# Kernel optimization log

Hardware: AMD Instinct MI355X
Metric: run time of the kernel (lower is better)

Reference implementation:

```python
import jax, jax.numpy as jnp
import numpy as np

B, N, D = 4, 2048, 1024
H, S, C, NSH, MV = 8, 3, 32, 3, 4


def _lin(key, fan_in, fan_out):
    k1, k2 = jax.random.split(key)
    lim = 1.0 / np.sqrt(fan_in)
    W = jax.random.uniform(k1, (fan_in, fan_out), minval=-lim, maxval=lim)
    b = jax.random.uniform(k2, (fan_out,), minval=-lim, maxval=lim)
    return W, b


def setup_inputs() -> dict:
    key = jax.random.key(0)
    ks = jax.random.split(key, 16)
    x = jax.random.normal(ks[0], (B, N, D), dtype=jnp.float32)
    W_sense, b_sense = _lin(ks[1], D, S * D)
    W_ctx, b_ctx = _lin(ks[2], D, D)
    W_sel, b_sel = _lin(ks[3], 2 * D, S)
    W_charge, b_charge = _lin(ks[4], D, 1)
    W_shell, b_shell = _lin(ks[5], D, NSH)
    W_class, b_class = _lin(ks[6], D, C)
    W_mass, b_mass = _lin(ks[7], D, 1)
    W_val, b_val = _lin(ks[8], D, MV)
    sparsity = 0.4
    init_val = -np.log(1.0 / sparsity - 1.0)
    compat_logits = jax.random.normal(ks[9], (C, C)) * 0.5 + init_val
    W_v, b_v = _lin(ks[10], D, D)
    W_out, b_out = _lin(ks[11], D, D)
    return {
        'x': x,
        'W_sense': W_sense, 'b_sense': b_sense,
        'W_ctx': W_ctx, 'b_ctx': b_ctx,
        'W_sel': W_sel, 'b_sel': b_sel,
        'W_charge': W_charge, 'b_charge': b_charge,
        'W_shell': W_shell, 'b_shell': b_shell,
        'W_class': W_class, 'b_class': b_class,
        'W_mass': W_mass, 'b_mass': b_mass,
        'W_val': W_val, 'b_val': b_val,
        'compat_logits': compat_logits.astype(jnp.float32),
        'w_charge': jnp.float32(1.0), 'w_shell': jnp.float32(0.5),
        'w_distance': jnp.float32(1.0), 'w_mass': jnp.float32(0.3),
        'w_valence': jnp.float32(0.3), 'temperature': jnp.float32(1.0),
        'W_v': W_v, 'b_v': b_v,
        'W_out': W_out, 'b_out': b_out,
    }


def reference(x, W_sense, b_sense, W_ctx, b_ctx, W_sel, b_sel,
              W_charge, b_charge, W_shell, b_shell, W_class, b_class,
              W_mass, b_mass, W_val, b_val, compat_logits,
              w_charge, w_shell, w_distance, w_mass, w_valence, temperature,
              W_v, b_v, W_out, b_out):
    b, n, d = x.shape
    sp = jax.nn.softplus

    # --- isotope selection (word-sense mixing) ---
    senses = (x @ W_sense + b_sense).reshape(b, n, S, d)          # (B,N,S,D)
    ctx_avg = (x @ W_ctx + b_ctx).mean(axis=1, keepdims=True)     # (B,1,D)
    sel_in = jnp.concatenate([x, jnp.broadcast_to(ctx_avg, (b, n, d))], axis=-1)
    sense_w = jax.nn.softmax(sel_in @ W_sel + b_sel, axis=-1)     # (B,N,S)
    x = jnp.einsum('bns,bnsd->bnd', sense_w, senses)

    # --- atomic properties ---
    charge = jnp.tanh(x @ W_charge + b_charge)[..., 0]            # (B,N)
    shell = jax.nn.softmax(x @ W_shell + b_shell, axis=-1)        # (B,N,NSH)
    cls = jnp.argmax(x @ W_class + b_class, axis=-1)              # (B,N) int
    mass = sp(x @ W_mass + b_mass)[..., 0] + 0.5                  # (B,N)
    val = jax.nn.softmax(x @ W_val + b_val, axis=-1)              # (B,N,MV)

    # --- class compatibility mask (B,N,N) ---
    compat = jax.nn.sigmoid((compat_logits + compat_logits.T) * 0.5)
    sparse_mask = compat[cls[:, :, None], cls[:, None, :]]

    # --- pairwise physics energy (B,N,N) ---
    pos = jnp.arange(n, dtype=x.dtype)
    dist = jnp.abs(pos[:, None] - pos[None, :])                   # (N,N)
    val_sum = val.sum(axis=-1)                                    # (B,N)
    E = (sp(w_charge) * charge[:, :, None] * charge[:, None, :]
         + sp(w_shell) * jnp.abs(shell[:, :, None, :] - shell[:, None, :, :]).sum(-1)
         - sp(w_distance) / (1.0 + 0.1 * dist)
         + sp(w_mass) * 0.1 * mass[:, :, None] * mass[:, None, :]
         - sp(w_valence) * (val_sum[:, :, None] + val_sum[:, None, :]) * 0.5)

    temp = sp(temperature)
    scores = (-E / temp) * sparse_mask
    causal = jnp.triu(jnp.ones((n, n), dtype=bool), k=1)
    scores = jnp.where(causal[None], -jnp.inf, scores)
    attn = jax.nn.softmax(scores, axis=-1)                        # (B,N,N)

    # --- weighted value aggregation (shared attn across heads) ---
    V = (x @ W_v + b_v).reshape(b, n, H, d // H)
    out = jnp.einsum('bij,bjhd->bihd', attn, V).reshape(b, n, d)
    return out @ W_out + b_out
```

## Files before the change

### kernel.cpp

```cpp
#include <hip/hip_runtime.h>
#include <hip/hip_bf16.h>
#include <cmath>

typedef __hip_bfloat16 bf16;
typedef __attribute__((ext_vector_type(4))) float floatx4;
typedef __attribute__((ext_vector_type(8))) short short8;
typedef __attribute__((ext_vector_type(8))) unsigned short ushort8;

__device__ __forceinline__ float bf2f(bf16 v) { return __bfloat162float(v); }
__device__ __forceinline__ bf16 f2bf(float v) { return __float2bfloat16(v); }
__device__ __forceinline__ float bfu2f(unsigned short u) { return __uint_as_float(((unsigned)u) << 16); }
__device__ __forceinline__ unsigned short f2bfu(float v) {
  bf16 h = __float2bfloat16(v);
  return __builtin_bit_cast(unsigned short, h);
}
__device__ __forceinline__ float softplusf(float x) {
  return x > 20.0f ? x : log1pf(expf(x));
}

__device__ __forceinline__ void async16(const void* g, void* l) {
  __builtin_amdgcn_global_load_lds(
      (const __attribute__((address_space(1))) unsigned int*)g,
      (__attribute__((address_space(3))) unsigned int*)l, 16, 0, 0);
}

template<int MODE, int CAUSAL, int ACCUM, int SWZ, int KSPLIT = 1>
__global__ __launch_bounds__(256) void gemm_bt(
    const bf16* __restrict__ A, const bf16* __restrict__ Bt,
    const float* __restrict__ bias, void* __restrict__ Cptr,
    int M, int N, int K, int lda, int ldb, int ldc,
    long aoffz, long boffz, long coffz)
{
  __shared__ __align__(16) bf16 As[2][128 * 64];
  __shared__ __align__(16) bf16 Bs[2][128 * 64];

  const int tid = threadIdx.x;
  const int lane = tid & 63;
  const int wave = tid >> 6;
  const int wr = wave >> 1, wc = wave & 1;
  const long z = blockIdx.z;
  int kstart = 0;
  long zz = z;
  if (KSPLIT > 1) {
    kstart = (int)(z % KSPLIT) * K;
    zz = z / KSPLIT;
  }
  A += zz * aoffz;
  Bt += zz * boffz;

  int bx, by;
  if (SWZ) {
    const int mtiles = M >> 7;
    const int per = mtiles >> 3;
    const int bid = (int)blockIdx.x;
    const int xcd = bid & 7;
    const int slot = bid >> 3;
    by = xcd * per + (slot % per);
    bx = slot / per;
  } else {
    bx = blockIdx.x;
    by = blockIdx.y;
  }
  const int m0 = by * 128, n0 = bx * 128;
  int kend = kstart + K;
  if (CAUSAL) {
    int klim = (by + 1) * 128;
    if (klim < kend) kend = klim;
  }

  int aoff[4], boff[4];
#pragma unroll
  for (int q = 0; q < 4; q++) {
    int ch = tid + 256 * q;
    int r = ch >> 3, c4 = ch & 7;
    int scol = (c4 ^ (r & 7)) * 8;
    aoff[q] = (m0 + r) * lda + scol;
    boff[q] = (n0 + r) * ldb + scol;
  }

  floatx4 acc[4][4] = {};
  const int fm = lane & 15, fq = lane >> 4;

  const int nt = (kend - kstart) >> 6;

#pragma unroll
  for (int q = 0; q < 4; q++) {
    int ch8 = (tid + 256 * q) * 8;
    async16(&A[(size_t)aoff[q] + kstart], &As[0][ch8]);
    async16(&Bt[(size_t)boff[q] + kstart], &Bs[0][ch8]);
  }
  __syncthreads();

  int cur = 0;
  for (int t = 0; t < nt; t++) {
    if (t + 1 < nt) {
      const int k0 = kstart + (t + 1) * 64;
#pragma unroll
      for (int q = 0; q < 4; q++) {
        int ch8 = (tid + 256 * q) * 8;
        async16(&A[(size_t)aoff[q] + k0], &As[cur ^ 1][ch8]);
        async16(&Bt[(size_t)boff[q] + k0], &Bs[cur ^ 1][ch8]);
      }
    }
#pragma unroll
    for (int kk = 0; kk < 2; kk++) {
      short8 af[4], bfr[4];
      const int c4 = fq + 4 * kk;
#pragma unroll
      for (int i = 0; i < 4; i++) {
        int R = wr * 64 + i * 16 + fm;
        af[i] = *(const short8*)&As[cur][(R * 8 + (c4 ^ (R & 7))) * 8];
      }
#pragma unroll
      for (int j = 0; j < 4; j++) {
        int R = wc * 64 + j * 16 + fm;
        bfr[j] = *(const short8*)&Bs[cur][(R * 8 + (c4 ^ (R & 7))) * 8];
      }
#pragma unroll
      for (int i = 0; i < 4; i++)
#pragma unroll
        for (int j = 0; j < 4; j++)
          acc[i][j] = __builtin_amdgcn_mfma_f32_16x16x32_bf16(af[i], bfr[j], acc[i][j], 0, 0, 0);
    }
    __syncthreads();
    cur ^= 1;
  }

  const int rm0 = (lane >> 4) * 4, cn = lane & 15;
#pragma unroll
  for (int i = 0; i < 4; i++) {
#pragma unroll
    for (int j = 0; j < 4; j++) {
      int nn = n0 + wc * 64 + j * 16 + cn;
      float bv = bias ? bias[nn] : 0.0f;
#pragma unroll
      for (int r = 0; r < 4; r++) {
        int mm = m0 + wr * 64 + i * 16 + rm0 + r;
        float v = acc[i][j][r] + bv;
        if (MODE == 0) {
          ((bf16*)Cptr)[z * coffz + (long)mm * ldc + nn] = f2bf(v);
        } else if (MODE == 1) {
          long idx = z * coffz + (long)mm * ldc + nn;
          float* Cf = (float*)Cptr;
          if (ACCUM) v += Cf[idx];
          Cf[idx] = v;
        } else {
          long idx = ((long)((mm >> 11) * 1024 + nn)) * 2048 + (mm & 2047);
          ((bf16*)Cptr)[idx] = f2bf(v);
        }
      }
    }
  }
}

__global__ __launch_bounds__(256) void gemm_y(
    const bf16* __restrict__ A, const bf16* __restrict__ Bt,
    const float* __restrict__ bsense, const float* __restrict__ sw,
    bf16* __restrict__ y)
{
  __shared__ __align__(16) bf16 As[2][128 * 64];
  __shared__ __align__(16) bf16 Bs[2][128 * 64];

  const int tid = threadIdx.x;
  const int lane = tid & 63;
  const int wave = tid >> 6;
  const int wr = wave >> 1, wc = wave & 1;

  const int bid = (int)blockIdx.x;
  const int xcd = bid & 7;
  const int slot = bid >> 3;
  const int by = xcd * 8 + (slot & 7);
  const int bx = slot >> 3;
  const int m0 = by * 128, n0 = bx * 128;

  int aoff[4], boff[4];
#pragma unroll
  for (int q = 0; q < 4; q++) {
    int ch = tid + 256 * q;
    int r = ch >> 3, c4 = ch & 7;
    int scol = (c4 ^ (r & 7)) * 8;
    aoff[q] = (m0 + r) * 3072 + scol;
    boff[q] = (n0 + r) * 3072 + scol;
  }

  floatx4 acc[4][4] = {};
  const int fm = lane & 15, fq = lane >> 4;

#pragma unroll
  for (int q = 0; q < 4; q++) {
    int ch8 = (tid + 256 * q) * 8;
    async16(&A[(size_t)aoff[q]], &As[0][ch8]);
    async16(&Bt[(size_t)boff[q]], &Bs[0][ch8]);
  }
  __syncthreads();

  int cur = 0;
  for (int t = 0; t < 48; t++) {
    if (t + 1 < 48) {
      const int k0 = (t + 1) * 64;
#pragma unroll
      for (int q = 0; q < 4; q++) {
        int ch8 = (tid + 256 * q) * 8;
        async16(&A[(size_t)aoff[q] + k0], &As[cur ^ 1][ch8]);
        async16(&Bt[(size_t)boff[q] + k0], &Bs[cur ^ 1][ch8]);
      }
    }
#pragma unroll
    for (int kk = 0; kk < 2; kk++) {
      short8 af[4], bfr[4];
      const int c4 = fq + 4 * kk;
#pragma unroll
      for (int i = 0; i < 4; i++) {
        int R = wr * 64 + i * 16 + fm;
        af[i] = *(const short8*)&As[cur][(R * 8 + (c4 ^ (R & 7))) * 8];
      }
#pragma unroll
      for (int j = 0; j < 4; j++) {
        int R = wc * 64 + j * 16 + fm;
        bfr[j] = *(const short8*)&Bs[cur][(R * 8 + (c4 ^ (R & 7))) * 8];
      }
#pragma unroll
      for (int i = 0; i < 4; i++)
#pragma unroll
        for (int j = 0; j < 4; j++)
          acc[i][j] = __builtin_amdgcn_mfma_f32_16x16x32_bf16(af[i], bfr[j], acc[i][j], 0, 0, 0);
    }
    __syncthreads();
    cur ^= 1;
  }

  const int rm0 = (lane >> 4) * 4, cn = lane & 15;
#pragma unroll
  for (int j = 0; j < 4; j++) {
    int nn = n0 + wc * 64 + j * 16 + cn;
    float b0 = bsense[nn], b1 = bsense[1024 + nn], b2 = bsense[2048 + nn];
#pragma unroll
    for (int i = 0; i < 4; i++) {
#pragma unroll
      for (int r = 0; r < 4; r++) {
        int mm = m0 + wr * 64 + i * 16 + rm0 + r;
        const float* sm = sw + (size_t)mm * 4;
        float v = acc[i][j][r] + sm[0] * b0 + sm[1] * b1 + sm[2] * b2;
        y[(size_t)mm * 1024 + nn] = f2bf(v);
      }
    }
  }
}

__global__ __launch_bounds__(256) void k_prescale(const float* __restrict__ x,
                                                  const float* __restrict__ sw,
                                                  bf16* __restrict__ Ap) {
  long id = (long)blockIdx.x * 256 + threadIdx.x;
  if (id >= 1048576L) return;
  int t = (int)(id >> 7);
  int kc = (int)(id & 127) << 3;
  const float* xt = x + (size_t)t * 1024 + kc;
  float4 a = *(const float4*)xt;
  float4 b = *(const float4*)(xt + 4);
  const float s0 = sw[t * 4 + 0], s1 = sw[t * 4 + 1], s2 = sw[t * 4 + 2];
  float v[8] = {a.x, a.y, a.z, a.w, b.x, b.y, b.z, b.w};
  ushort8 o0, o1, o2;
#pragma unroll
  for (int e = 0; e < 8; e++) {
    o0[e] = f2bfu(s0 * v[e]);
    o1[e] = f2bfu(s1 * v[e]);
    o2[e] = f2bfu(s2 * v[e]);
  }
  bf16* row = Ap + (size_t)t * 3072 + kc;
  *(ushort8*)(row) = o0;
  *(ushort8*)(row + 1024) = o1;
  *(ushort8*)(row + 2048) = o2;
}

__global__ __launch_bounds__(256) void k_split_x3(const float* __restrict__ x,
                                                  bf16* __restrict__ xhhl) {
  long id = (long)blockIdx.x * 256 + threadIdx.x;
  if (id >= 8388608L) return;
  long t = id >> 10;
  int d = (int)(id & 1023);
  float v = x[id];
  bf16 h = f2bf(v);
  bf16 l = f2bf(v - bf2f(h));
  bf16* row = xhhl + t * 3072;
  row[d] = h;
  row[1024 + d] = h;
  row[2048 + d] = l;
}

__global__ __launch_bounds__(256) void k_split_ws3(const float* __restrict__ Ws,
                                                   bf16* __restrict__ Wsn3) {
  long id = (long)blockIdx.x * 256 + threadIdx.x;
  if (id >= 3145728L) return;
  int row10 = (int)(id >> 10);
  int d = row10 / 3;
  int s = row10 - d * 3;
  int dp = (int)(id & 1023);
  float v = Ws[id];
  bf16 h = f2bf(v);
  bf16 l = f2bf(v - bf2f(h));
  bf16* row = Wsn3 + ((size_t)(s * 1024 + d)) * 3072;
  row[dp] = h;
  row[1024 + dp] = l;
  row[2048 + dp] = h;
}

__global__ __launch_bounds__(256) void k_trans_hl(const float* __restrict__ src,
                                                  bf16* __restrict__ dh,
                                                  int R, int C) {
  __shared__ float tile[32][33];
  int c0 = blockIdx.x * 32, r0 = blockIdx.y * 32;
  int tx = threadIdx.x & 31, ty = threadIdx.x >> 5;
  for (int rr = ty; rr < 32; rr += 8)
    tile[rr][tx] = src[(size_t)(r0 + rr) * C + c0 + tx];
  __syncthreads();
  for (int rr = ty; rr < 32; rr += 8)
    dh[(size_t)(c0 + rr) * R + r0 + tx] = f2bf(tile[tx][rr]);
}

__global__ __launch_bounds__(256) void k_trans_sense(const float* __restrict__ Ws,
                                                     bf16* __restrict__ Bt2) {
  __shared__ float tile[32][33];
  int c0 = blockIdx.x * 32, r0 = blockIdx.y * 32, s = blockIdx.z;
  int tx = threadIdx.x & 31, ty = threadIdx.x >> 5;
  for (int rr = ty; rr < 32; rr += 8)
    tile[rr][tx] = Ws[(size_t)(r0 + rr) * 3072 + s * 1024 + c0 + tx];
  __syncthreads();
  for (int rr = ty; rr < 32; rr += 8)
    Bt2[(size_t)(c0 + rr) * 3072 + s * 1024 + r0 + tx] = f2bf(tile[tx][rr]);
}

__global__ __launch_bounds__(256) void k_pack(
    const float* __restrict__ W_charge, const float* __restrict__ W_shell,
    const float* __restrict__ W_class, const float* __restrict__ W_mass,
    const float* __restrict__ b_charge, const float* __restrict__ b_shell,
    const float* __restrict__ b_class, const float* __restrict__ b_mass,
    const float* __restrict__ compat_logits,
    bf16* __restrict__ Whhl3, float* __restrict__ bhead, float* __restrict__ csig)
{
  int c = blockIdx.x;
  int tid = threadIdx.x;
  for (int e = tid; e < 1024; e += 256) {
    float v;
    if (c == 0) v = W_charge[e];
    else if (c < 4) v = W_shell[e * 3 + (c - 1)];
    else if (c == 4) v = W_mass[e];
    else if (c < 37) v = W_class[e * 32 + (c - 5)];
    else v = 0.0f;
    bf16 h = f2bf(v);
    bf16 l = f2bf(v - bf2f(h));
    bf16* row = Whhl3 + (size_t)c * 3072;
    row[e] = h;
    row[1024 + e] = h;
    row[2048 + e] = l;
  }
  if (c == 0 && tid < 37) {
    float v;
    if (tid == 0) v = b_charge[0];
    else if (tid < 4) v = b_shell[tid - 1];
    else if (tid == 4) v = b_mass[0];
    else v = b_class[tid - 5];
    bhead[tid] = v;
  }
  if (c == 1) {
    for (int k = tid; k < 1024; k += 256) {
      int ii = k >> 5, jj = k & 31;
      float l = 0.5f * (compat_logits[ii * 32 + jj] + compat_logits[jj * 32 + ii]);
      csig[k] = 1.0f / (1.0f + expf(-l));
    }
  }
}

__global__ __launch_bounds__(256) void k_bh(
    const float* __restrict__ b_sense, const float* __restrict__ W_charge,
    const float* __restrict__ W_shell, const float* __restrict__ W_class,
    const float* __restrict__ W_mass, float* __restrict__ bh)
{
  const int c = blockIdx.x, s = blockIdx.y;
  const int tid = threadIdx.x;
  __shared__ float red[256];
  float p = 0.0f;
  for (int e = tid; e < 1024; e += 256) {
    float w;
    if (c == 0) w = W_charge[e];
    else if (c < 4) w = W_shell[e * 3 + (c - 1)];
    else if (c == 4) w = W_mass[e];
    else w = W_class[e * 32 + (c - 5)];
    p += b_sense[s * 1024 + e] * w;
  }
  red[tid] = p;
  __syncthreads();
  for (int st = 128; st > 0; st >>= 1) {
    if (tid < st) red[tid] += red[tid + st];
    __syncthreads();
  }
  if (tid == 0) bh[s * 128 + c] = red[0];
}

__global__ __launch_bounds__(256) void k_reduce_mt(const float* __restrict__ Mtp,
                                                   float* __restrict__ Mt) {
  long o = (long)blockIdx.x * 256 + threadIdx.x;
  if (o >= 393216L) return;
  long s = o >> 17;
  long i = o & 131071;
  const float* p = Mtp + s * 8 * 131072 + i;
  float acc = 0.0f;
#pragma unroll
  for (int kc = 0; kc < 8; kc++) acc += p[(size_t)kc * 131072];
  Mt[o] = acc;
}

__global__ __launch_bounds__(256) void k_split(const float* __restrict__ Mt,
                                               const float* __restrict__ W_sel,
                                               bf16* __restrict__ Mthl) {
  long id = (long)blockIdx.x * 256 + threadIdx.x;
  if (id >= 1572864L) return;
  int n = (int)(id / 3072);
  int k = (int)(id - (long)n * 3072);
  int third = k >> 10;
  int j = k & 1023;
  float v;
  if (n < 384) {
    v = Mt[(size_t)n * 1024 + j];
  } else {
    int c2 = n - 384;
    v = (c2 < 3) ? W_sel[(size_t)j * 3 + c2] : 0.0f;
  }
  bf16 h = f2bf(v);
  Mthl[id] = (third == 1) ? f2bf(v - bf2f(h)) : h;
}

__global__ __launch_bounds__(256) void k_xbar(const float* __restrict__ x, float* __restrict__ xbar) {
  const int d = blockIdx.x * 256 + threadIdx.x;
  const int b = blockIdx.y;
  const int n0 = blockIdx.z * 256;
  const float* xb = x + (size_t)b * 2048 * 1024 + (size_t)n0 * 1024 + d;
  float s = 0.0f;
  for (int n = 0; n < 256; n++) s += xb[(size_t)n * 1024];
  atomicAdd(&xbar[b * 1024 + d], s * (1.0f / 2048.0f));
}

__global__ __launch_bounds__(256) void k_q(const float* __restrict__ W_ctx,
                                           const float* __restrict__ b_ctx,
                                           const float* __restrict__ W_sel,
                                           float* __restrict__ q) {
  const int e = blockIdx.x;
  const int tid = threadIdx.x;
  const float* row = (e < 1024) ? (W_ctx + (size_t)e * 1024) : b_ctx;
  float p0 = 0.0f, p1 = 0.0f, p2 = 0.0f;
  for (int d = tid; d < 1024; d += 256) {
    float v = row[d];
    const float* ws = W_sel + (size_t)(1024 + d) * 3;
    p0 += v * ws[0]; p1 += v * ws[1]; p2 += v * ws[2];
  }
  __shared__ float red[3][256];
  red[0][tid] = p0; red[1][tid] = p1; red[2][tid] = p2;
  __syncthreads();
  for (int st = 128; st > 0; st >>= 1) {
    if (tid < st) {
      red[0][tid] += red[0][tid + st];
      red[1][tid] += red[1][tid + st];
      red[2][tid] += red[2][tid + st];
    }
    __syncthreads();
  }
  if (tid < 3) q[(size_t)e * 3 + tid] = red[tid][0];
}

__global__ __launch_bounds__(256) void k_ctxsel(const float* __restrict__ xbar,
                                                const float* __restrict__ q,
                                                float* __restrict__ ctx_sel) {
  const int b = blockIdx.x;
  const int tid = threadIdx.x;
  float p0 = 0.0f, p1 = 0.0f, p2 = 0.0f;
  for (int e = tid; e < 1024; e += 256) {
    float v = xbar[b * 1024 + e];
    p0 += v * q[e * 3 + 0]; p1 += v * q[e * 3 + 1]; p2 += v * q[e * 3 + 2];
  }
  __shared__ float red[3][256];
  red[0][tid] = p0; red[1][tid] = p1; red[2][tid] = p2;
  __syncthreads();
  for (int st = 128; st > 0; st >>= 1) {
    if (tid < st) {
      red[0][tid] += red[0][tid + st];
      red[1][tid] += red[1][tid + st];
      red[2][tid] += red[2][tid + st];
    }
    __syncthreads();
  }
  if (tid < 3) ctx_sel[b * 3 + tid] = red[tid][0] + q[1024 * 3 + tid];
}

__global__ __launch_bounds__(64) void k_heads(
    const float* __restrict__ H, const float* __restrict__ ctx_sel,
    const float* __restrict__ b_sel, const float* __restrict__ bh,
    const float* __restrict__ bhead,
    float* __restrict__ sw, float* __restrict__ feat)
{
  const int t = blockIdx.x;
  const int b = t >> 11;
  const int lane = threadIdx.x;
  const float* Ht = H + (size_t)t * 512;
  const float* Ht2 = H + 4194304 + (size_t)t * 512;

  float s0 = Ht[384] + Ht2[384] + ctx_sel[b * 3 + 0] + b_sel[0];
  float s1 = Ht[385] + Ht2[385] + ctx_sel[b * 3 + 1] + b_sel[1];
  float s2 = Ht[386] + Ht2[386] + ctx_sel[b * 3 + 2] + b_sel[2];
  float mx = fmaxf(s0, fmaxf(s1, s2));
  float e0 = expf(s0 - mx), e1 = expf(s1 - mx), e2 = expf(s2 - mx);
  float inv = 1.0f / (e0 + e1 + e2);
  float w0 = e0 * inv, w1 = e1 * inv, w2 = e2 * inv;

  __shared__ float L[64];
  if (lane < 37) {
    float lg = bhead[lane];
    lg += w0 * (Ht[lane] + Ht2[lane] + bh[lane]);
    lg += w1 * (Ht[128 + lane] + Ht2[128 + lane] + bh[128 + lane]);
    lg += w2 * (Ht[256 + lane] + Ht2[256 + lane] + bh[256 + lane]);
    L[lane] = lg;
  }
  __syncthreads();
  if (lane == 0) {
    float charge = tanhf(L[0]);
    float h0 = L[1], h1 = L[2], h2 = L[3];
    float hm = fmaxf(h0, fmaxf(h1, h2));
    float x0 = expf(h0 - hm), x1 = expf(h1 - hm), x2 = expf(h2 - hm);
    float hinv = 1.0f / (x0 + x1 + x2);
    float mass = softplusf(L[4]) + 0.5f;
    int cls = 0;
    float best = L[5];
    for (int c = 1; c < 32; c++) {
      if (L[5 + c] > best) { best = L[5 + c]; cls = c; }
    }
    float* f = feat + (size_t)t * 8;
    f[0] = charge; f[1] = mass;
    f[2] = x0 * hinv; f[3] = x1 * hinv; f[4] = x2 * hinv;
    f[5] = (float)cls; f[6] = 0.0f; f[7] = 0.0f;
    float* sp_ = sw + (size_t)t * 4;
    sp_[0] = w0; sp_[1] = w1; sp_[2] = w2; sp_[3] = 0.0f;
  }
}

__global__ __launch_bounds__(256) void k_scores(
    const float* __restrict__ feat, const float* __restrict__ compat,
    const float* __restrict__ wchg, const float* __restrict__ wsh,
    const float* __restrict__ wdist, const float* __restrict__ wmass,
    const float* __restrict__ wval, const float* __restrict__ temp_p,
    bf16* __restrict__ P)
{
  const int i = blockIdx.x, b = blockIdx.y;
  const int tid = threadIdx.x;
  __shared__ float cs[1024];
  __shared__ float red[256];
  for (int k = tid; k < 1024; k += 256) cs[k] = compat[k];
  __syncthreads();

  const float a = softplusf(wchg[0]);
  const float bs = softplusf(wsh[0]);
  const float c = softplusf(wdist[0]);
  const float dm = softplusf(wmass[0]);
  const float ev = softplusf(wval[0]);
  const float itmp = 1.0f / softplusf(temp_p[0]);

  const float4* fi4 = (const float4*)(feat + ((size_t)b * 2048 + i) * 8);
  float4 fiA = fi4[0], fiB = fi4[1];
  const float ci = fiA.x, mi = fiA.y, si0 = fiA.z, si1 = fiA.w, si2 = fiB.x;
  int cli = (int)fiB.y; cli = cli < 0 ? 0 : (cli > 31 ? 31 : cli);

  float sc[8];
  float lmax = -3.0e38f;
#pragma unroll
  for (int jj = 0; jj < 8; jj++) {
    int j = tid + jj * 256;
    const float4* fj4 = (const float4*)(feat + ((size_t)b * 2048 + j) * 8);
    float4 fjA = fj4[0], fjB = fj4[1];
    int clj = (int)fjB.y; clj = clj < 0 ? 0 : (clj > 31 ? 31 : clj);
    float E = a * ci * fjA.x
            + bs * (fabsf(si0 - fjA.z) + fabsf(si1 - fjA.w) + fabsf(si2 - fjB.x))
            - c / (1.0f + 0.1f * fabsf((float)(i - j)))
            + dm * 0.1f * mi * fjA.y
            - ev;
    float s = (j <= i) ? (-E * itmp) * cs[cli * 32 + clj] : -3.0e38f;
    sc[jj] = s;
    lmax = fmaxf(lmax, s);
  }
  red[tid] = lmax;
  __syncthreads();
  for (int st = 128; st > 0; st >>= 1) {
    if (tid < st) red[tid] = fmaxf(red[tid], red[tid + st]);
    __syncthreads();
  }
  const float mrow = red[0];
  __syncthreads();

  float pv[8];
  float lsum = 0.0f;
#pragma unroll
  for (int jj = 0; jj < 8; jj++) {
    pv[jj] = (sc[jj] > -1.0e37f) ? expf(sc[jj] - mrow) : 0.0f;
    lsum += pv[jj];
  }
  red[tid] = lsum;
  __syncthreads();
  for (int st = 128; st > 0; st >>= 1) {
    if (tid < st) red[tid] += red[tid + st];
    __syncthreads();
  }
  const float inv = 1.0f / red[0];
  bf16* Pi = P + ((size_t)b * 2048 + i) * 2048;
#pragma unroll
  for (int jj = 0; jj < 8; jj++) Pi[tid + jj * 256] = f2bf(pv[jj] * inv);
}

extern "C" void kernel_launch(void* const* d_in, const int* in_sizes, int n_in,
                              void* d_out, int out_size, void* d_ws, size_t ws_size,
                              hipStream_t stream) {
  (void)in_sizes; (void)n_in; (void)out_size; (void)ws_size;
  const float* x        = (const float*)d_in[0];
  const float* W_sense  = (const float*)d_in[1];
  const float* b_sense  = (const float*)d_in[2];
  const float* W_ctx    = (const float*)d_in[3];
  const float* b_ctx    = (const float*)d_in[4];
  const float* W_sel    = (const float*)d_in[5];
  const float* b_sel    = (const float*)d_in[6];
  const float* W_charge = (const float*)d_in[7];
  const float* b_charge = (const float*)d_in[8];
  const float* W_shell  = (const float*)d_in[9];
  const float* b_shell  = (const float*)d_in[10];
  const float* W_class  = (const float*)d_in[11];
  const float* b_class  = (const float*)d_in[12];
  const float* W_mass   = (const float*)d_in[13];
  const float* b_mass   = (const float*)d_in[14];
  const float* compat_logits = (const float*)d_in[17];
  const float* w_charge = (const float*)d_in[18];
  const float* w_shell  = (const float*)d_in[19];
  const float* w_distance = (const float*)d_in[20];
  const float* w_mass   = (const float*)d_in[21];
  const float* w_valence = (const float*)d_in[22];
  const float* temperature = (const float*)d_in[23];
  const float* W_v      = (const float*)d_in[24];
  const float* b_v      = (const float*)d_in[25];
  const float* W_out    = (const float*)d_in[26];
  const float* b_out    = (const float*)d_in[27];

  char* w = (char*)d_ws;
  auto alloc = [&](size_t bytes) {
    char* p = w;
    w += (bytes + 255) & ~(size_t)255;
    return p;
  };
  bf16* xhhl  = (bf16*)alloc(8192ULL * 3072 * 2);
  char* R1    = alloc(48ULL * 1024 * 1024);
  bf16* Wsn3  = (bf16*)R1;
  float* Hh   = (float*)R1;
  float* Mtp  = (float*)(R1 + 20ULL * 1024 * 1024);
  bf16* Mthl  = (bf16*)(R1 + 40ULL * 1024 * 1024);
  float* Mt   = (float*)(R1 + 44ULL * 1024 * 1024);
  bf16* y     = (bf16*)R1;
  bf16* Wts2  = (bf16*)alloc(3072ULL * 1024 * 2);
  bf16* Wt_v  = (bf16*)alloc(1024ULL * 1024 * 2);
  bf16* Wt_out = (bf16*)alloc(1024ULL * 1024 * 2);
  bf16* Whhl3 = (bf16*)alloc(128ULL * 3072 * 2);
  float* bh   = (float*)alloc(3ULL * 128 * 4);
  float* bhead = (float*)alloc(256);
  float* csig = (float*)alloc(4096);
  float* xbar = (float*)alloc(4ULL * 1024 * 4);
  float* qbuf = (float*)alloc(1025ULL * 3 * 4);
  float* ctx_sel = (float*)alloc(256);
  float* feat = (float*)alloc(8192ULL * 8 * 4);
  float* sw   = (float*)alloc(8192ULL * 4 * 4);
  bf16* Aprime = xhhl;
  bf16* Vt = xhhl + 8388608;
  bf16* O  = xhhl + 16777216;
  bf16* P  = (bf16*)d_out;

  k_split_x3<<<32768, 256, 0, stream>>>(x, xhhl);
  k_split_ws3<<<12288, 256, 0, stream>>>(W_sense, Wsn3);
  k_trans_sense<<<dim3(32, 32, 3), 256, 0, stream>>>(W_sense, Wts2);
  k_trans_hl<<<dim3(32, 32), 256, 0, stream>>>(W_v, Wt_v, 1024, 1024);
  k_trans_hl<<<dim3(32, 32), 256, 0, stream>>>(W_out, Wt_out, 1024, 1024);
  k_pack<<<128, 256, 0, stream>>>(W_charge, W_shell, W_class, W_mass,
                                  b_charge, b_shell, b_class, b_mass,
                                  compat_logits, Whhl3, bhead, csig);

  hipMemsetAsync(xbar, 0, 4096 * 4, stream);
  k_xbar<<<dim3(4, 4, 8), 256, 0, stream>>>(x, xbar);
  k_q<<<1025, 256, 0, stream>>>(W_ctx, b_ctx, W_sel, qbuf);
  k_ctxsel<<<4, 256, 0, stream>>>(xbar, qbuf, ctx_sel);

  gemm_bt<1, 0, 0, 0, 8><<<dim3(8, 1, 24), 256, 0, stream>>>(
      Whhl3, Wsn3, nullptr, Mtp, 128, 1024, 384, 3072, 3072, 1024,
      0, 3145728L, 131072L);
  k_reduce_mt<<<1536, 256, 0, stream>>>(Mtp, Mt);
  k_split<<<6144, 256, 0, stream>>>(Mt, W_sel, Mthl);

  gemm_bt<1, 0, 0, 1, 2><<<dim3(256, 1, 2), 256, 0, stream>>>(
      xhhl, Mthl, nullptr, Hh, 8192, 512, 1536, 3072, 3072, 512,
      0, 0, 4194304L);

  k_bh<<<dim3(37, 3), 256, 0, stream>>>(b_sense, W_charge, W_shell, W_class, W_mass, bh);
  k_heads<<<8192, 64, 0, stream>>>(Hh, ctx_sel, b_sel, bh, bhead, sw, feat);

  k_prescale<<<4096, 256, 0, stream>>>(x, sw, Aprime);

  gemm_y<<<512, 256, 0, stream>>>(Aprime, Wts2, b_sense, sw, y);

  gemm_bt<2, 0, 0, 1><<<512, 256, 0, stream>>>(
      y, Wt_v, b_v, Vt, 8192, 1024, 1024, 1024, 1024, 0, 0, 0, 0);

  k_scores<<<dim3(2048, 4), 256, 0, stream>>>(feat, csig, w_charge, w_shell,
                                              w_distance, w_mass, w_valence, temperature, P);

  gemm_bt<0, 1, 0, 0><<<dim3(8, 16, 4), 256, 0, stream>>>(
      P, Vt, nullptr, O, 2048, 1024, 2048, 2048, 2048, 1024,
      2048L * 2048, 1024L * 2048, 2048L * 1024);

  gemm_bt<1, 0, 0, 1><<<512, 256, 0, stream>>>(
      O, Wt_out, b_out, (float*)d_out, 8192, 1024, 1024, 1024, 1024, 1024, 0, 0, 0);
}
```

Baseline: 546.3 us.

## Switch GEMMs to 3-stage BK=32 LDS pipeline with vmcnt waits and causal reorder

Both GEMM kernels move from a double-buffered 64-wide K tile to a triple-buffered 32-wide K tile with a new LDS swizzle. Each iteration now waits only for the previous stage with explicit s_waitcnt vmcnt plus s_barrier, so global loads stay in flight across iterations. LDS use drops to 48KB per block and launch bounds ask for 3 blocks per CU to raise occupancy. Causal GEMMs also reverse the row-block order so the longest tiles launch first, at the cost of twice as many barriers per unit of K.

```diff
diff --git a/kernel.cpp b/kernel.cpp
--- a/kernel.cpp
+++ b/kernel.cpp
@@ -25,14 +25,14 @@
 }
 
 template<int MODE, int CAUSAL, int ACCUM, int SWZ, int KSPLIT = 1>
-__global__ __launch_bounds__(256) void gemm_bt(
+__global__ __launch_bounds__(256, 3) void gemm_bt(
     const bf16* __restrict__ A, const bf16* __restrict__ Bt,
     const float* __restrict__ bias, void* __restrict__ Cptr,
     int M, int N, int K, int lda, int ldb, int ldc,
     long aoffz, long boffz, long coffz)
 {
-  __shared__ __align__(16) bf16 As[2][128 * 64];
-  __shared__ __align__(16) bf16 Bs[2][128 * 64];
+  __shared__ __align__(16) bf16 As[3][128 * 32];
+  __shared__ __align__(16) bf16 Bs[3][128 * 32];
 
   const int tid = threadIdx.x;
   const int lane = tid & 63;
@@ -60,6 +60,7 @@
   } else {
     bx = blockIdx.x;
     by = blockIdx.y;
+    if (CAUSAL) by = (int)gridDim.y - 1 - by;
   }
   const int m0 = by * 128, n0 = bx * 128;
   int kend = kstart + K;
@@ -68,62 +69,60 @@
     if (klim < kend) kend = klim;
   }
 
-  int aoff[4], boff[4];
-#pragma unroll
-  for (int q = 0; q < 4; q++) {
-    int ch = tid + 256 * q;
-    int r = ch >> 3, c4 = ch & 7;
-    int scol = (c4 ^ (r & 7)) * 8;
-    aoff[q] = (m0 + r) * lda + scol;
-    boff[q] = (n0 + r) * ldb + scol;
-  }
+  const int ch0 = tid, ch1 = tid + 256;
+  const int sw0 = ((ch0 & 3) ^ ((ch0 >> 3) & 3)) * 8;
+  const int sw1 = ((ch1 & 3) ^ ((ch1 >> 3) & 3)) * 8;
+  const size_t a0 = (size_t)(m0 + (ch0 >> 2)) * lda + sw0;
+  const size_t a1 = (size_t)(m0 + (ch1 >> 2)) * lda + sw1;
+  const size_t b0 = (size_t)(n0 + (ch0 >> 2)) * ldb + sw0;
+  const size_t b1 = (size_t)(n0 + (ch1 >> 2)) * ldb + sw1;
 
   floatx4 acc[4][4] = {};
   const int fm = lane & 15, fq = lane >> 4;
-
-  const int nt = (kend - kstart) >> 6;
-
-#pragma unroll
-  for (int q = 0; q < 4; q++) {
-    int ch8 = (tid + 256 * q) * 8;
-    async16(&A[(size_t)aoff[q] + kstart], &As[0][ch8]);
-    async16(&Bt[(size_t)boff[q] + kstart], &Bs[0][ch8]);
-  }
-  __syncthreads();
-
-  int cur = 0;
+  const int gph = (fm >> 1) & 3;
+  const int nt = (kend - kstart) >> 5;
+
+  auto stage = [&](int buf, int t) {
+    const int k0 = kstart + t * 32;
+    async16(&A[a0 + k0], &As[buf][ch0 * 8]);
+    async16(&A[a1 + k0], &As[buf][ch1 * 8]);
+    async16(&Bt[b0 + k0], &Bs[buf][ch0 * 8]);
+    async16(&Bt[b1 + k0], &Bs[buf][ch1 * 8]);
+  };
+
+  stage(0, 0);
+  if (nt > 1) {
+    stage(1, 1);
+    asm volatile("s_waitcnt vmcnt(4)" ::: "memory");
+  } else {
+    asm volatile("s_waitcnt vmcnt(0)" ::: "memory");
+  }
+  asm volatile("s_barrier" ::: "memory");
+
+  int bufc = 0;
   for (int t = 0; t < nt; t++) {
-    if (t + 1 < nt) {
-      const int k0 = kstart + (t + 1) * 64;
-#pragma unroll
-      for (int q = 0; q < 4; q++) {
-        int ch8 = (tid + 256 * q) * 8;
-        async16(&A[(size_t)aoff[q] + k0], &As[cur ^ 1][ch8]);
-        async16(&Bt[(size_t)boff[q] + k0], &Bs[cur ^ 1][ch8]);
-      }
-    }
-#pragma unroll
-    for (int kk = 0; kk < 2; kk++) {
-      short8 af[4], bfr[4];
-      const int c4 = fq + 4 * kk;
-#pragma unroll
-      for (int i = 0; i < 4; i++) {
-        int R = wr * 64 + i * 16 + fm;
-        af[i] = *(const short8*)&As[cur][(R * 8 + (c4 ^ (R & 7))) * 8];
-      }
-#pragma unroll
-      for (int j = 0; j < 4; j++) {
-        int R = wc * 64 + j * 16 + fm;
-        bfr[j] = *(const short8*)&Bs[cur][(R * 8 + (c4 ^ (R & 7))) * 8];
-      }
-#pragma unroll
-      for (int i = 0; i < 4; i++)
-#pragma unroll
-        for (int j = 0; j < 4; j++)
-          acc[i][j] = __builtin_amdgcn_mfma_f32_16x16x32_bf16(af[i], bfr[j], acc[i][j], 0, 0, 0);
-    }
-    __syncthreads();
-    cur ^= 1;
+    int bufn = bufc + 2; if (bufn >= 3) bufn -= 3;
+    if (t + 2 < nt) stage(bufn, t + 2);
+    short8 af[4], bfr[4];
+#pragma unroll
+    for (int i = 0; i < 4; i++) {
+      int R = wr * 64 + i * 16 + fm;
+      af[i] = *(const short8*)&As[bufc][R * 32 + ((fq ^ gph) << 3)];
+    }
+#pragma unroll
+    for (int j = 0; j < 4; j++) {
+      int R = wc * 64 + j * 16 + fm;
+      bfr[j] = *(const short8*)&Bs[bufc][R * 32 + ((fq ^ gph) << 3)];
+    }
+#pragma unroll
+    for (int i = 0; i < 4; i++)
+#pragma unroll
+      for (int j = 0; j < 4; j++)
+        acc[i][j] = __builtin_amdgcn_mfma_f32_16x16x32_bf16(af[i], bfr[j], acc[i][j], 0, 0, 0);
+    if (t + 2 < nt) asm volatile("s_waitcnt vmcnt(4)" ::: "memory");
+    else            asm volatile("s_waitcnt vmcnt(0)" ::: "memory");
+    asm volatile("s_barrier" ::: "memory");
+    bufc++; if (bufc == 3) bufc = 0;
   }
 
   const int rm0 = (lane >> 4) * 4, cn = lane & 15;
@@ -153,13 +152,13 @@
   }
 }
 
-__global__ __launch_bounds__(256) void gemm_y(
+__global__ __launch_bounds__(256, 3) void gemm_y(
     const bf16* __restrict__ A, const bf16* __restrict__ Bt,
     const float* __restrict__ bsense, const float* __restrict__ sw,
     bf16* __restrict__ y)
 {
-  __shared__ __align__(16) bf16 As[2][128 * 64];
-  __shared__ __align__(16) bf16 Bs[2][128 * 64];
+  __shared__ __align__(16) bf16 As[3][128 * 32];
+  __shared__ __align__(16) bf16 Bs[3][128 * 32];
 
   const int tid = threadIdx.x;
   const int lane = tid & 63;
@@ -173,74 +172,69 @@
   const int bx = slot >> 3;
   const int m0 = by * 128, n0 = bx * 128;
 
-  int aoff[4], boff[4];
-#pragma unroll
-  for (int q = 0; q < 4; q++) {
-    int ch = tid + 256 * q;
-    int r = ch >> 3, c4 = ch & 7;
-    int scol = (c4 ^ (r & 7)) * 8;
-    aoff[q] = (m0 + r) * 3072 + scol;
-    boff[q] = (n0 + r) * 3072 + scol;
-  }
+  const int ch0 = tid, ch1 = tid + 256;
+  const int sw0 = ((ch0 & 3) ^ ((ch0 >> 3) & 3)) * 8;
+  const int sw1 = ((ch1 & 3) ^ ((ch1 >> 3) & 3)) * 8;
+  const size_t a0 = (size_t)(m0 + (ch0 >> 2)) * 3072 + sw0;
+  const size_t a1 = (size_t)(m0 + (ch1 >> 2)) * 3072 + sw1;
+  const size_t b0 = (size_t)(n0 + (ch0 >> 2)) * 3072 + sw0;
+  const size_t b1 = (size_t)(n0 + (ch1 >> 2)) * 3072 + sw1;
 
   floatx4 acc[4][4] = {};
   const int fm = lane & 15, fq = lane >> 4;
-
-#pragma unroll
-  for (int q = 0; q < 4; q++) {
-    int ch8 = (tid + 256 * q) * 8;
-    async16(&A[(size_t)aoff[q]], &As[0][ch8]);
-    async16(&Bt[(size_t)boff[q]], &Bs[0][ch8]);
-  }
-  __syncthreads();
-
-  int cur = 0;
-  for (int t = 0; t < 48; t++) {
-    if (t + 1 < 48) {
-      const int k0 = (t + 1) * 64;
-#pragma unroll
-      for (int q = 0; q < 4; q++) {
-        int ch8 = (tid + 256 * q) * 8;
-        async16(&A[(size_t)aoff[q] + k0], &As[cur ^ 1][ch8]);
-        async16(&Bt[(size_t)boff[q] + k0], &Bs[cur ^ 1][ch8]);
-      }
-    }
-#pragma unroll
-    for (int kk = 0; kk < 2; kk++) {
-      short8 af[4], bfr[4];
-      const int c4 = fq + 4 * kk;
-#pragma unroll
-      for (int i = 0; i < 4; i++) {
-        int R = wr * 64 + i * 16 + fm;
-        af[i] = *(const short8*)&As[cur][(R * 8 + (c4 ^ (R & 7))) * 8];
-      }
-#pragma unroll
-      for (int j = 0; j < 4; j++) {
-        int R = wc * 64 + j * 16 + fm;
-        bfr[j] = *(const short8*)&Bs[cur][(R * 8 + (c4 ^ (R & 7))) * 8];
-      }
-#pragma unroll
-      for (int i = 0; i < 4; i++)
-#pragma unroll
-        for (int j = 0; j < 4; j++)
-          acc[i][j] = __builtin_amdgcn_mfma_f32_16x16x32_bf16(af[i], bfr[j], acc[i][j], 0, 0, 0);
-    }
-    __syncthreads();
-    cur ^= 1;
+  const int gph = (fm >> 1) & 3;
+
+  auto stage = [&](int buf, int t) {
+    const int k0 = t * 32;
+    async16(&A[a0 + k0], &As[buf][ch0 * 8]);
+    async16(&A[a1 + k0], &As[buf][ch1 * 8]);
+    async16(&Bt[b0 + k0], &Bs[buf][ch0 * 8]);
+    async16(&Bt[b1 + k0], &Bs[buf][ch1 * 8]);
+  };
+
+  stage(0, 0);
+  stage(1, 1);
+  asm volatile("s_waitcnt vmcnt(4)" ::: "memory");
+  asm volatile("s_barrier" ::: "memory");
+
+  int bufc = 0;
+  for (int t = 0; t < 96; t++) {
+    int bufn = bufc + 2; if (bufn >= 3) bufn -= 3;
+    if (t + 2 < 96) stage(bufn, t + 2);
+    short8 af[4], bfr[4];
+#pragma unroll
+    for (int i = 0; i < 4; i++) {
+      int R = wr * 64 + i * 16 + fm;
+      af[i] = *(const short8*)&As[bufc][R * 32 + ((fq ^ gph) << 3)];
+    }
+#pragma unroll
+    for (int j = 0; j < 4; j++) {
+      int R = wc * 64 + j * 16 + fm;
+      bfr[j] = *(const short8*)&Bs[bufc][R * 32 + ((fq ^ gph) << 3)];
+    }
+#pragma unroll
+    for (int i = 0; i < 4; i++)
+#pragma unroll
+      for (int j = 0; j < 4; j++)
+        acc[i][j] = __builtin_amdgcn_mfma_f32_16x16x32_bf16(af[i], bfr[j], acc[i][j], 0, 0, 0);
+    if (t + 2 < 96) asm volatile("s_waitcnt vmcnt(4)" ::: "memory");
+    else            asm volatile("s_waitcnt vmcnt(0)" ::: "memory");
+    asm volatile("s_barrier" ::: "memory");
+    bufc++; if (bufc == 3) bufc = 0;
   }
 
   const int rm0 = (lane >> 4) * 4, cn = lane & 15;
 #pragma unroll
   for (int j = 0; j < 4; j++) {
     int nn = n0 + wc * 64 + j * 16 + cn;
-    float b0 = bsense[nn], b1 = bsense[1024 + nn], b2 = bsense[2048 + nn];
+    float bb0 = bsense[nn], bb1 = bsense[1024 + nn], bb2 = bsense[2048 + nn];
 #pragma unroll
     for (int i = 0; i < 4; i++) {
 #pragma unroll
       for (int r = 0; r < 4; r++) {
         int mm = m0 + wr * 64 + i * 16 + rm0 + r;
         const float* sm = sw + (size_t)mm * 4;
-        float v = acc[i][j][r] + sm[0] * b0 + sm[1] * b1 + sm[2] * b2;
+        float v = acc[i][j][r] + sm[0] * bb0 + sm[1] * bb1 + sm[2] * bb2;
         y[(size_t)mm * 1024 + nn] = f2bf(v);
       }
     }
```

New measurement: 542.4 us. No clear change (-0.7%).
